# Kernel optimization log

Hardware: AMD Instinct MI355X
Metric: run time of the kernel (lower is better)

## Reference

```python
import jax, jax.numpy as jnp
import numpy as np

ROPE_BASE = 100.0  # CroCo RoPE2D default freq


def _rope1d(tok, pos):
    # tok: [B, H, N, D], pos: [B, N] int
    D = tok.shape[-1]
    inv_freq = 1.0 / (ROPE_BASE ** (jnp.arange(0, D, 2, dtype=jnp.float32) / D))
    ang = pos[..., None].astype(jnp.float32) * inv_freq          # [B, N, D/2]
    cos = jnp.concatenate([jnp.cos(ang), jnp.cos(ang)], -1)[:, None]  # [B,1,N,D]
    sin = jnp.concatenate([jnp.sin(ang), jnp.sin(ang)], -1)[:, None]
    x1, x2 = jnp.split(tok, 2, axis=-1)
    rot = jnp.concatenate([-x2, x1], -1)
    return tok * cos.astype(tok.dtype) + rot * sin.astype(tok.dtype)


def _rope2d(tok, pos):
    # first half of head channels rotated with y coords, second half with x
    t_y, t_x = jnp.split(tok, 2, axis=-1)
    return jnp.concatenate([_rope1d(t_y, pos[..., 0]), _rope1d(t_x, pos[..., 1])], -1)


def setup_inputs() -> dict:
    key0 = jax.random.key(0)
    ks = jax.random.split(key0, 10)
    B, Nq, Nk, C, H = 4, 2048, 2048, 1024, 16
    s = 1.0 / np.sqrt(C)
    return {
        "query": jax.random.normal(ks[0], (B, Nq, C), jnp.float32),
        "key": jax.random.normal(ks[1], (B, Nk, C), jnp.float32),
        "value": jax.random.normal(ks[2], (B, Nk, C), jnp.float32),
        "qpos": jax.random.randint(ks[3], (B, Nq, 2), 0, 64),
        "kpos": jax.random.randint(ks[4], (B, Nk, 2), 0, 64),
        "Wq": jax.random.normal(ks[5], (C, C), jnp.float32) * s,
        "Wk": jax.random.normal(ks[6], (C, C), jnp.float32) * s,
        "Wv": jax.random.normal(ks[7], (C, C), jnp.float32) * s,
        "Wo": jax.random.normal(ks[8], (C, C), jnp.float32) * s,
        "bo": jax.random.normal(ks[9], (C,), jnp.float32) * 0.01,
    }


def reference(query, key, value, qpos, kpos, Wq, Wk, Wv, Wo, bo):
    B, Nq, C = query.shape
    H = 16
    D = C // H
    scale = D ** (-0.5)
    # separate Q/K/V projections (torch Linear: x @ W.T), split into heads
    q = (query @ Wq.T).reshape(B, Nq, H, D).transpose(0, 2, 1, 3)
    k = (key @ Wk.T).reshape(B, key.shape[1], H, D).transpose(0, 2, 1, 3)
    v = (value @ Wv.T).reshape(B, value.shape[1], H, D).transpose(0, 2, 1, 3)
    # inline fp16 cast around RoPE, as in the original
    q = _rope2d(q.astype(jnp.float16), qpos).astype(jnp.float32)
    k = _rope2d(k.astype(jnp.float16), kpos).astype(jnp.float32)
    # SDPA
    scores = jnp.einsum("bhqd,bhkd->bhqk", q, k) * scale
    attn = jax.nn.softmax(scores, axis=-1)
    x = jnp.einsum("bhqk,bhkd->bhqd", attn, v)
    x = x.transpose(0, 2, 1, 3).reshape(B, Nq, C)
    return x @ Wo.T + bo
```

## Files before the change

### kernel.cpp

```cpp
#include <hip/hip_runtime.h>
#include <math.h>

typedef _Float16 half_t;
typedef __attribute__((ext_vector_type(8))) _Float16 f16x8;
typedef __attribute__((ext_vector_type(4))) float f32x4;

#define MFMA16(a, b, c) __builtin_amdgcn_mfma_f32_16x16x32_f16((a), (b), (c), 0, 0, 0)

constexpr int Bc = 4, NQ = 2048, NKC = 2048, CC = 1024, NHD = 16, HDIM = 64;

__device__ __forceinline__ void async_copy16(half_t* lds, const half_t* g) {
  __builtin_amdgcn_global_load_lds(
      (const __attribute__((address_space(1))) unsigned*)g,
      (__attribute__((address_space(3))) unsigned*)lds, 16, 0, 0);
}

__global__ __launch_bounds__(256) void cvt16(const float* __restrict__ src,
                                             half_t* __restrict__ dst) {
  const int i = blockIdx.x * 256 + threadIdx.x;
  const f32x4 a = ((const f32x4*)src)[2 * i];
  const f32x4 b = ((const f32x4*)src)[2 * i + 1];
  f16x8 h;
#pragma unroll
  for (int j = 0; j < 4; ++j) { h[j] = (half_t)a[j]; h[4 + j] = (half_t)b[j]; }
  ((f16x8*)dst)[i] = h;
}

__global__ __launch_bounds__(256) void cvtW(const float* __restrict__ s0,
                                            const float* __restrict__ s1,
                                            const float* __restrict__ s2,
                                            const float* __restrict__ s3,
                                            half_t* __restrict__ dst) {
  const int y = blockIdx.y;
  const float* src = (y == 0) ? s0 : (y == 1) ? s1 : (y == 2) ? s2 : s3;
  const int i = blockIdx.x * 256 + threadIdx.x;
  const f32x4 a = ((const f32x4*)src)[2 * i];
  const f32x4 b = ((const f32x4*)src)[2 * i + 1];
  f16x8 h;
#pragma unroll
  for (int j = 0; j < 4; ++j) { h[j] = (half_t)a[j]; h[4 + j] = (half_t)b[j]; }
  ((f16x8*)(dst + (size_t)y * CC * CC))[i] = h;
}

template <bool FINAL>
__global__ __launch_bounds__(256) void gemm_lds(const half_t* __restrict__ X,
                                                const half_t* __restrict__ W,
                                                half_t* __restrict__ out16,
                                                float* __restrict__ outf,
                                                const float* __restrict__ bias) {
  __shared__ half_t As[128 * 32];
  __shared__ half_t Bs[128 * 32];
  const int tid  = threadIdx.x;
  const int wave = tid >> 6, lane = tid & 63;
  const int quad = lane >> 4, l16 = lane & 15;
  const int m0 = blockIdx.y * 128, n0 = blockIdx.x * 128;
  const int mw = (wave >> 1) * 64, nw = (wave & 1) * 64;

  const int srow = lane >> 2, skoff = (lane & 3) * 8;
  const half_t* xa = X + (size_t)(m0 + wave * 32 + srow) * CC + skoff;
  const half_t* xb = W + (size_t)(n0 + wave * 32 + srow) * CC + skoff;
  half_t* lA0 = &As[(wave * 2 + 0) * 512];
  half_t* lA1 = &As[(wave * 2 + 1) * 512];
  half_t* lB0 = &Bs[(wave * 2 + 0) * 512];
  half_t* lB1 = &Bs[(wave * 2 + 1) * 512];

  f32x4 acc[4][4] = {};

  for (int k0 = 0; k0 < CC; k0 += 32) {
    __syncthreads();
    async_copy16(lA0, xa + k0);
    async_copy16(lA1, xa + 16 * CC + k0);
    async_copy16(lB0, xb + k0);
    async_copy16(lB1, xb + 16 * CC + k0);
    __syncthreads();

    f16x8 af[4], bf[4];
#pragma unroll
    for (int mi = 0; mi < 4; ++mi) af[mi] = *(const f16x8*)&As[(mw + mi * 16 + l16) * 32 + quad * 8];
#pragma unroll
    for (int ni = 0; ni < 4; ++ni) bf[ni] = *(const f16x8*)&Bs[(nw + ni * 16 + l16) * 32 + quad * 8];
#pragma unroll
    for (int mi = 0; mi < 4; ++mi)
#pragma unroll
      for (int ni = 0; ni < 4; ++ni) acc[mi][ni] = MFMA16(af[mi], bf[ni], acc[mi][ni]);
  }

#pragma unroll
  for (int mi = 0; mi < 4; ++mi)
#pragma unroll
    for (int ni = 0; ni < 4; ++ni)
#pragma unroll
      for (int r = 0; r < 4; ++r) {
        const size_t row = (size_t)(m0 + mw + mi * 16 + quad * 4 + r);
        const size_t col = (size_t)(n0 + nw + ni * 16 + l16);
        if constexpr (FINAL) outf[row * CC + col] = acc[mi][ni][r] + bias[col];
        else                 out16[row * CC + col] = (half_t)acc[mi][ni][r];
      }
}

__global__ __launch_bounds__(256) void rope_kernel(half_t* __restrict__ t,
                                                   const int* __restrict__ pos) {
#pragma clang fp contract(off)
  const int gid = blockIdx.x * 256 + threadIdx.x;
  const int i       = gid & 15;
  const int halfsel = (gid >> 4) & 1;
  const int h       = (gid >> 5) & 15;
  const int n       = (gid >> 9) & 2047;
  const int b       = gid >> 20;

  const int p = pos[((b * NQ + n) << 1) + halfsel];
  const float inv = __builtin_amdgcn_exp2f((float)i * -0.41524100904865773f);
  const float ang = (float)p * inv;
  const half_t hc = (half_t)cosf(ang);
  const half_t hs = (half_t)sinf(ang);

  const size_t base = (size_t)(b * NQ + n) * CC + h * HDIM + halfsel * 32;
  const half_t t1 = t[base + i];
  const half_t t2 = t[base + 16 + i];
  const half_t p1 = t1 * hc;
  const half_t p2 = t2 * hs;
  const half_t p3 = t2 * hc;
  const half_t p4 = t1 * hs;
  t[base + i]      = p1 - p2;
  t[base + 16 + i] = p3 + p4;
}

__global__ __launch_bounds__(256, 4) void attn_kernel(const half_t* __restrict__ q16,
                                                      const half_t* __restrict__ k16,
                                                      const half_t* __restrict__ v16,
                                                      half_t* __restrict__ x16) {
  __shared__ half_t Ksf[4 * 64 * 16];
  __shared__ half_t Vt[64][72];
  __shared__ half_t Pl[4][32][72];
  const int tid  = threadIdx.x;
  const int wave = tid >> 6, lane = tid & 63;
  const int quad = lane >> 4, l16 = lane & 15;
  const int qblk = blockIdx.x, h = blockIdx.y, b = blockIdx.z;
  const f32x4 zero = {0.f, 0.f, 0.f, 0.f};

  f16x8 qa[2][2];
  {
    const half_t* qbase =
        q16 + (size_t)(b * NQ + qblk * 128 + wave * 32 + l16) * CC + h * HDIM + quad * 8;
#pragma unroll
    for (int mi = 0; mi < 2; ++mi)
#pragma unroll
      for (int kc = 0; kc < 2; ++kc)
        qa[mi][kc] = *(const f16x8*)(qbase + (size_t)mi * 16 * CC + kc * 32);
  }

  f32x4 o[2][4] = {};
  f32x4 lp[2] = {};

  const int skey = tid >> 2, sd0 = (tid & 3) * 16;
  const int vp = tid & 31, vd0 = (tid >> 5) * 8;
  const half_t* kptr = k16 + (size_t)(b * NKC + skey) * CC + h * HDIM + sd0;
  const half_t* vptr = v16 + (size_t)(b * NKC + 2 * vp) * CC + h * HDIM + vd0;

  int kdst[2];
#pragma unroll
  for (int c = 0; c < 2; ++c) {
    const int d = sd0 + 8 * c;
    const int nb = skey >> 4, kc = d >> 5, qd = (d & 31) >> 3;
    const int slot = (skey & 15) + 16 * qd;
    kdst[c] = (nb * 64 + slot) * 16 + kc * 8;
  }

  f16x8 kr0, kr1, vr0, vr1;
  kr0 = *(const f16x8*)kptr;
  kr1 = *(const f16x8*)(kptr + 8);
  vr0 = *(const f16x8*)vptr;
  vr1 = *(const f16x8*)(vptr + CC);

  for (int kt = 0; kt < NKC; kt += 64) {
    __syncthreads();
    *(f16x8*)&Ksf[kdst[0]] = kr0;
    *(f16x8*)&Ksf[kdst[1]] = kr1;
#pragma unroll
    for (int i = 0; i < 8; ++i) {
      union { half_t h2[2]; unsigned u; } pk;
      pk.h2[0] = vr0[i]; pk.h2[1] = vr1[i];
      *(unsigned*)&Vt[vd0 + i][2 * vp] = pk.u;
    }
    __syncthreads();

    if (kt + 64 < NKC) {
      const half_t* kn = kptr + (size_t)(kt + 64) * CC;
      const half_t* vn = vptr + (size_t)(kt + 64) * CC;
      kr0 = *(const f16x8*)kn;
      kr1 = *(const f16x8*)(kn + 8);
      vr0 = *(const f16x8*)vn;
      vr1 = *(const f16x8*)(vn + CC);
    }

    f32x4 s[2][4];
#pragma unroll
    for (int nb = 0; nb < 4; ++nb) {
      const f16x8 kb0 = *(const f16x8*)&Ksf[(nb * 64 + lane) * 16 + 0];
      const f16x8 kb1 = *(const f16x8*)&Ksf[(nb * 64 + lane) * 16 + 8];
#pragma unroll
      for (int mi = 0; mi < 2; ++mi) {
        const f32x4 t0 = MFMA16(qa[mi][0], kb0, zero);
        s[mi][nb] = MFMA16(qa[mi][1], kb1, t0);
      }
    }

#pragma unroll
    for (int mi = 0; mi < 2; ++mi)
#pragma unroll
      for (int nb = 0; nb < 4; ++nb)
#pragma unroll
        for (int r = 0; r < 4; ++r) {
          const float p = __builtin_amdgcn_exp2f(s[mi][nb][r] * 0.18033688011112042f);
          s[mi][nb][r] = p;
          lp[mi][r] += p;
        }

#pragma unroll
    for (int mi = 0; mi < 2; ++mi)
#pragma unroll
      for (int nb = 0; nb < 4; ++nb)
#pragma unroll
        for (int r = 0; r < 4; ++r)
          Pl[wave][mi * 16 + quad * 4 + r][nb * 16 + l16] = (half_t)s[mi][nb][r];

#pragma unroll
    for (int kc = 0; kc < 2; ++kc) {
      const f16x8 pa0 = *(const f16x8*)&Pl[wave][l16][kc * 32 + quad * 8];
      const f16x8 pa1 = *(const f16x8*)&Pl[wave][16 + l16][kc * 32 + quad * 8];
#pragma unroll
      for (int nd = 0; nd < 4; ++nd) {
        const f16x8 vb = *(const f16x8*)&Vt[nd * 16 + l16][kc * 32 + quad * 8];
        o[0][nd] = MFMA16(pa0, vb, o[0][nd]);
        o[1][nd] = MFMA16(pa1, vb, o[1][nd]);
      }
    }
  }

#pragma unroll
  for (int mi = 0; mi < 2; ++mi)
#pragma unroll
    for (int r = 0; r < 4; ++r) {
      float rs = lp[mi][r];
#pragma unroll
      for (int off = 1; off < 16; off <<= 1) rs += __shfl_xor(rs, off);
      const float inv = 1.f / rs;
      const size_t row =
          (size_t)(b * NQ + qblk * 128 + wave * 32 + mi * 16 + quad * 4 + r) * CC + h * HDIM;
#pragma unroll
      for (int nd = 0; nd < 4; ++nd)
        x16[row + nd * 16 + l16] = (half_t)(o[mi][nd][r] * inv);
    }
}

extern "C" void kernel_launch(void* const* d_in, const int* in_sizes, int n_in,
                              void* d_out, int out_size, void* d_ws, size_t ws_size,
                              hipStream_t stream) {
  const float* query = (const float*)d_in[0];
  const float* key   = (const float*)d_in[1];
  const float* value = (const float*)d_in[2];
  const int*   qpos  = (const int*)d_in[3];
  const int*   kpos  = (const int*)d_in[4];
  const float* Wq = (const float*)d_in[5];
  const float* Wk = (const float*)d_in[6];
  const float* Wv = (const float*)d_in[7];
  const float* Wo = (const float*)d_in[8];
  const float* bo = (const float*)d_in[9];
  float* out = (float*)d_out;

  const size_t NT = (size_t)Bc * NQ * CC;
  half_t* q16 = (half_t*)d_ws;
  half_t* k16 = q16 + NT;
  half_t* v16 = k16 + NT;
  half_t* A0  = v16 + NT;
  half_t* W16 = A0 + NT;
  half_t* x16 = A0;

  const int nbA = (int)(NT / 8 / 256);
  const int nbW = (CC * CC) / 8 / 256;

  cvtW<<<dim3(nbW, 4), 256, 0, stream>>>(Wq, Wk, Wv, Wo, W16);

  const dim3 gg(CC / 128, Bc * NQ / 128);
  cvt16<<<nbA, 256, 0, stream>>>(query, A0);
  gemm_lds<false><<<gg, 256, 0, stream>>>(A0, W16 + 0 * (size_t)CC * CC, q16, nullptr, nullptr);
  cvt16<<<nbA, 256, 0, stream>>>(key, A0);
  gemm_lds<false><<<gg, 256, 0, stream>>>(A0, W16 + 1 * (size_t)CC * CC, k16, nullptr, nullptr);
  cvt16<<<nbA, 256, 0, stream>>>(value, A0);
  gemm_lds<false><<<gg, 256, 0, stream>>>(A0, W16 + 2 * (size_t)CC * CC, v16, nullptr, nullptr);

  rope_kernel<<<(Bc * NQ * NHD * 32) / 256, 256, 0, stream>>>(q16, qpos);
  rope_kernel<<<(Bc * NQ * NHD * 32) / 256, 256, 0, stream>>>(k16, kpos);

  attn_kernel<<<dim3(NQ / 128, NHD, Bc), 256, 0, stream>>>(q16, k16, v16, x16);

  gemm_lds<true><<<gg, 256, 0, stream>>>(x16, W16 + 3 * (size_t)CC * CC, nullptr, out, bo);
}
```

Baseline: 406.0 us.

## Transpose attention MFMA operands and swizzle LDS layouts for P and V

Swaps the MFMA operand order so the score and output tiles are computed transposed (keys/head-dim as rows, queries as columns). Each lane then owns a single query row, which lets the row sum be one scalar per lane and the output be written as packed 4-wide stores. P is staged in a smaller XOR-swizzled LDS buffer one 16-row slice at a time, and V is stored in a swizzled fragment layout. The aim is fewer LDS bank conflicts, less LDS traffic and footprint, and fewer scalar stores, at the cost of more complex indexing that could be wrong.

```diff
diff --git a/kernel.cpp b/kernel.cpp
--- a/kernel.cpp
+++ b/kernel.cpp
@@ -3,6 +3,7 @@
 
 typedef _Float16 half_t;
 typedef __attribute__((ext_vector_type(8))) _Float16 f16x8;
+typedef __attribute__((ext_vector_type(4))) _Float16 f16x4;
 typedef __attribute__((ext_vector_type(4))) float f32x4;
 
 #define MFMA16(a, b, c) __builtin_amdgcn_mfma_f32_16x16x32_f16((a), (b), (c), 0, 0, 0)
@@ -129,12 +130,14 @@
                                                       const half_t* __restrict__ k16,
                                                       const half_t* __restrict__ v16,
                                                       half_t* __restrict__ x16) {
-  __shared__ half_t Ksf[4 * 64 * 16];
-  __shared__ half_t Vt[64][72];
-  __shared__ half_t Pl[4][32][72];
+  __shared__ __align__(16) half_t Kf[4 * 2 * 64 * 8];
+  __shared__ __align__(16) unsigned Vfd[2 * 4 * 64 * 4];
+  __shared__ __align__(16) unsigned Pb[4][16][32];
+
   const int tid  = threadIdx.x;
   const int wave = tid >> 6, lane = tid & 63;
   const int quad = lane >> 4, l16 = lane & 15;
+  const int lx   = lane ^ quad;
   const int qblk = blockIdx.x, h = blockIdx.y, b = blockIdx.z;
   const f32x4 zero = {0.f, 0.f, 0.f, 0.f};
 
@@ -150,21 +153,24 @@
   }
 
   f32x4 o[2][4] = {};
-  f32x4 lp[2] = {};
+  float lp[2] = {};
 
   const int skey = tid >> 2, sd0 = (tid & 3) * 16;
-  const int vp = tid & 31, vd0 = (tid >> 5) * 8;
   const half_t* kptr = k16 + (size_t)(b * NKC + skey) * CC + h * HDIM + sd0;
-  const half_t* vptr = v16 + (size_t)(b * NKC + 2 * vp) * CC + h * HDIM + vd0;
-
   int kdst[2];
 #pragma unroll
   for (int c = 0; c < 2; ++c) {
     const int d = sd0 + 8 * c;
-    const int nb = skey >> 4, kc = d >> 5, qd = (d & 31) >> 3;
-    const int slot = (skey & 15) + 16 * qd;
-    kdst[c] = (nb * 64 + slot) * 16 + kc * 8;
-  }
+    const int kc = d >> 5, qd = (d & 31) >> 3;
+    kdst[c] = ((((skey >> 4) * 2 + kc) * 64) + qd * 16 + (skey & 15)) * 8;
+  }
+
+  const int vp = tid & 31, vd0 = (tid >> 5) * 8;
+  const half_t* vptr = v16 + (size_t)(b * NKC + 2 * vp) * CC + h * HDIM + vd0;
+  const int vkc = vp >> 4, vqd = (vp & 15) >> 2, vnd = vd0 >> 4;
+  const int vl16b = vd0 & 15;
+  const int vswz  = vqd ^ (vkc << 2);
+  const int vbase = ((vkc * 4 + vnd) * 64 + vqd * 16) * 4 + (vp & 3);
 
   f16x8 kr0, kr1, vr0, vr1;
   kr0 = *(const f16x8*)kptr;
@@ -174,13 +180,13 @@
 
   for (int kt = 0; kt < NKC; kt += 64) {
     __syncthreads();
-    *(f16x8*)&Ksf[kdst[0]] = kr0;
-    *(f16x8*)&Ksf[kdst[1]] = kr1;
+    *(f16x8*)&Kf[kdst[0]] = kr0;
+    *(f16x8*)&Kf[kdst[1]] = kr1;
 #pragma unroll
     for (int i = 0; i < 8; ++i) {
       union { half_t h2[2]; unsigned u; } pk;
       pk.h2[0] = vr0[i]; pk.h2[1] = vr1[i];
-      *(unsigned*)&Vt[vd0 + i][2 * vp] = pk.u;
+      Vfd[vbase + (((vl16b + i) ^ vswz) << 2)] = pk.u;
     }
     __syncthreads();
 
@@ -193,64 +199,58 @@
       vr1 = *(const f16x8*)(vn + CC);
     }
 
-    f32x4 s[2][4];
-#pragma unroll
-    for (int nb = 0; nb < 4; ++nb) {
-      const f16x8 kb0 = *(const f16x8*)&Ksf[(nb * 64 + lane) * 16 + 0];
-      const f16x8 kb1 = *(const f16x8*)&Ksf[(nb * 64 + lane) * 16 + 8];
-#pragma unroll
-      for (int mi = 0; mi < 2; ++mi) {
-        const f32x4 t0 = MFMA16(qa[mi][0], kb0, zero);
-        s[mi][nb] = MFMA16(qa[mi][1], kb1, t0);
-      }
-    }
-
-#pragma unroll
-    for (int mi = 0; mi < 2; ++mi)
-#pragma unroll
-      for (int nb = 0; nb < 4; ++nb)
+#pragma unroll
+    for (int mi = 0; mi < 2; ++mi) {
+      f32x4 st[4];
+#pragma unroll
+      for (int kb = 0; kb < 4; ++kb) {
+        const f16x8 ka0 = *(const f16x8*)&Kf[((kb * 2 + 0) * 64 + lane) * 8];
+        const f16x8 ka1 = *(const f16x8*)&Kf[((kb * 2 + 1) * 64 + lane) * 8];
+        const f32x4 t0 = MFMA16(ka0, qa[mi][0], zero);
+        st[kb] = MFMA16(ka1, qa[mi][1], t0);
+      }
+
+#pragma unroll
+      for (int kb = 0; kb < 4; ++kb) {
+        f16x4 w;
 #pragma unroll
         for (int r = 0; r < 4; ++r) {
-          const float p = __builtin_amdgcn_exp2f(s[mi][nb][r] * 0.18033688011112042f);
-          s[mi][nb][r] = p;
-          lp[mi][r] += p;
+          const float p = __builtin_amdgcn_exp2f(st[kb][r] * 0.18033688011112042f);
+          lp[mi] += p;
+          w[r] = (half_t)p;
         }
-
-#pragma unroll
-    for (int mi = 0; mi < 2; ++mi)
-#pragma unroll
-      for (int nb = 0; nb < 4; ++nb)
-#pragma unroll
-        for (int r = 0; r < 4; ++r)
-          Pl[wave][mi * 16 + quad * 4 + r][nb * 16 + l16] = (half_t)s[mi][nb][r];
-
-#pragma unroll
-    for (int kc = 0; kc < 2; ++kc) {
-      const f16x8 pa0 = *(const f16x8*)&Pl[wave][l16][kc * 32 + quad * 8];
-      const f16x8 pa1 = *(const f16x8*)&Pl[wave][16 + l16][kc * 32 + quad * 8];
-#pragma unroll
-      for (int nd = 0; nd < 4; ++nd) {
-        const f16x8 vb = *(const f16x8*)&Vt[nd * 16 + l16][kc * 32 + quad * 8];
-        o[0][nd] = MFMA16(pa0, vb, o[0][nd]);
-        o[1][nd] = MFMA16(pa1, vb, o[1][nd]);
-      }
-    }
-  }
-
-#pragma unroll
-  for (int mi = 0; mi < 2; ++mi)
-#pragma unroll
-    for (int r = 0; r < 4; ++r) {
-      float rs = lp[mi][r];
-#pragma unroll
-      for (int off = 1; off < 16; off <<= 1) rs += __shfl_xor(rs, off);
-      const float inv = 1.f / rs;
-      const size_t row =
-          (size_t)(b * NQ + qblk * 128 + wave * 32 + mi * 16 + quad * 4 + r) * CC + h * HDIM;
-#pragma unroll
-      for (int nd = 0; nd < 4; ++nd)
-        x16[row + nd * 16 + l16] = (half_t)(o[mi][nd][r] * inv);
-    }
+        const int m0 = kb * 8 + quad * 2;
+        *(f16x4*)&Pb[wave][l16][m0 ^ ((l16 & 7) << 2)] = w;
+      }
+
+#pragma unroll
+      for (int kc = 0; kc < 2; ++kc) {
+        const f16x8 pa = *(const f16x8*)&Pb[wave][l16][(kc * 16 + quad * 4) ^ ((l16 & 7) << 2)];
+#pragma unroll
+        for (int nd = 0; nd < 4; ++nd) {
+          const f16x8 vb = *(const f16x8*)&Vfd[(((kc * 4 + nd) * 64) + (lx ^ (kc << 2))) * 4];
+          o[mi][nd] = MFMA16(vb, pa, o[mi][nd]);
+        }
+      }
+    }
+  }
+
+#pragma unroll
+  for (int mi = 0; mi < 2; ++mi) {
+    float rs = lp[mi];
+    rs += __shfl_xor(rs, 16);
+    rs += __shfl_xor(rs, 32);
+    const float inv = 1.f / rs;
+    const size_t row =
+        (size_t)(b * NQ + qblk * 128 + wave * 32 + mi * 16 + l16) * CC + h * HDIM;
+#pragma unroll
+    for (int nd = 0; nd < 4; ++nd) {
+      f16x4 w;
+#pragma unroll
+      for (int r = 0; r < 4; ++r) w[r] = (half_t)(o[mi][nd][r] * inv);
+      *(f16x4*)&x16[row + nd * 16 + quad * 4] = w;
+    }
+  }
 }
 
 extern "C" void kernel_launch(void* const* d_in, const int* in_sizes, int n_in,
```

Result: slower. 643.8 us (+58.6%).
